# Kernel tuning notes

Hardware: AMD Instinct MI355X
Metric: run time of the kernel (lower is better)

Reference implementation:

```python
import jax, jax.numpy as jnp
import numpy as np

DIM = 512
HEADS = 8
HEAD_DIM = DIM // HEADS
EPS = 1e-5

def _ln(x, g, b):
    m = jnp.mean(x, axis=-1, keepdims=True)
    v = jnp.mean((x - m) ** 2, axis=-1, keepdims=True)
    return (x - m) * jax.lax.rsqrt(v + EPS) * g + b

def setup_inputs() -> dict:
    key = jax.random.key(0)
    ks = jax.random.split(key, 12)
    s = 0.02
    d, dff = DIM, 4 * DIM
    inp = {
        'x': jax.random.normal(ks[0], (8, 4096, d), jnp.float32),
        'Wq': jax.random.normal(ks[1], (d, d), jnp.float32) * s,
        'bq': jnp.zeros((d,), jnp.float32),
        'Wk': jax.random.normal(ks[2], (d, d), jnp.float32) * s,
        'bk': jnp.zeros((d,), jnp.float32),
        'Wv': jax.random.normal(ks[3], (d, d), jnp.float32) * s,
        'bv': jnp.zeros((d,), jnp.float32),
        'Wo': jax.random.normal(ks[4], (d, d), jnp.float32) * s,
        'bo': jnp.zeros((d,), jnp.float32),
        'g1': jnp.ones((d,), jnp.float32),
        'b1': jnp.zeros((d,), jnp.float32),
        'g2': jnp.ones((d,), jnp.float32),
        'b2': jnp.zeros((d,), jnp.float32),
        'Wf1': jax.random.normal(ks[5], (d, dff), jnp.float32) * s,
        'bf1': jnp.zeros((dff,), jnp.float32),
        'Wf2': jax.random.normal(ks[6], (dff, d), jnp.float32) * s,
        'bf2': jnp.zeros((d,), jnp.float32),
    }
    return inp

def _linear_attn(x, Wq, bq, Wk, bk, Wv, bv, Wo, bo):
    b, n, d = x.shape
    def split(t):
        return t.reshape(b, n, HEADS, HEAD_DIM).transpose(0, 2, 1, 3)  # bhnd
    q = split(x @ Wq + bq)
    k = split(x @ Wk + bk)
    v = split(x @ Wv + bv)
    q = jax.nn.elu(q) + 1.0
    k = jax.nn.elu(k) + 1.0
    kv = jnp.einsum('bhnd,bhnf->bhdf', k, v)
    out = jnp.einsum('bhnd,bhdf->bhnf', q, kv)
    out = out.transpose(0, 2, 1, 3).reshape(b, n, d)
    return out @ Wo + bo

def reference(x, Wq, bq, Wk, bk, Wv, bv, Wo, bo, g1, b1, g2, b2, Wf1, bf1, Wf2, bf2):
    # series decomposition: AvgPool1d(k=3, stride=1, pad=1, count_include_pad=True)
    xp = jnp.pad(x, ((0, 0), (1, 1), (0, 0)))
    trend = (xp[:, :-2] + xp[:, 1:-1] + xp[:, 2:]) / 3.0
    seasonal = x - trend
    seasonal = seasonal + _linear_attn(_ln(seasonal, g1, b1), Wq, bq, Wk, bk, Wv, bv, Wo, bo)
    h = _ln(seasonal, g2, b2)
    h = jax.nn.gelu(h @ Wf1 + bf1, approximate=False) @ Wf2 + bf2
    seasonal = seasonal + h
    return seasonal + trend
```

## Files before the change

### kernel.cpp

```cpp
#include <hip/hip_runtime.h>
#include <math.h>

typedef __bf16 bf16;
typedef __attribute__((ext_vector_type(8))) __bf16 bf16x8;
typedef __attribute__((ext_vector_type(4))) float floatx4;

#define DIM 512
#define DFF 2048
#define SEQ 4096
#define ROWS 32768

#define GLOBAL_AS(p) ((const __attribute__((address_space(1))) void*)(p))
#define LDS_AS(p)    ((__attribute__((address_space(3))) void*)(p))

__global__ __launch_bounds__(256) void prep_w_kernel(const float* __restrict__ W,
                                                     bf16* __restrict__ Wt, int K, int N)
{
    int idx = blockIdx.x * 256 + threadIdx.x;
    if (idx >= K * N) return;
    int k = idx % K;
    int n = idx / K;
    Wt[idx] = (bf16)W[(size_t)k * N + n];
}

__global__ __launch_bounds__(256) void prep_w3_kernel(const float* __restrict__ Wq,
                                                      const float* __restrict__ Wk,
                                                      const float* __restrict__ Wv,
                                                      bf16* __restrict__ Wt)
{
    int idx = blockIdx.x * 256 + threadIdx.x;
    int which = idx >> 18;
    int r = idx & 262143;
    int k = r & 511;
    int n = r >> 9;
    const float* W = (which == 0) ? Wq : (which == 1 ? Wk : Wv);
    Wt[idx] = (bf16)W[(size_t)k * 512 + n];
}

__global__ __launch_bounds__(256) void pack_bias_kernel(const float* __restrict__ bq,
                                                        const float* __restrict__ bk,
                                                        const float* __restrict__ bv,
                                                        float* __restrict__ out)
{
    int i = blockIdx.x * 256 + threadIdx.x;
    if (i >= 1536) return;
    out[i] = (i < 512) ? bq[i] : (i < 1024 ? bk[i - 512] : bv[i - 1024]);
}

__device__ inline float wave_red(float v)
{
#pragma unroll
    for (int off = 32; off; off >>= 1) v += __shfl_xor(v, off, 64);
    return v;
}

__global__ __launch_bounds__(256) void decomp_ln_kernel(const float* __restrict__ x,
                                                        const float* __restrict__ g,
                                                        const float* __restrict__ be,
                                                        float* __restrict__ S,
                                                        bf16* __restrict__ XN)
{
    int wave = threadIdx.x >> 6, lane = threadIdx.x & 63;
    int r = blockIdx.x * 4 + wave;
    int n = r & (SEQ - 1);
    const float4* xr = (const float4*)(x + (size_t)r * DIM);
    float4 z = make_float4(0.f, 0.f, 0.f, 0.f);
    float s[8];
#pragma unroll
    for (int i = 0; i < 2; ++i) {
        int c4 = lane * 2 + i;
        float4 v0 = xr[c4];
        float4 vm = (n > 0)       ? xr[c4 - DIM / 4] : z;
        float4 vp = (n < SEQ - 1) ? xr[c4 + DIM / 4] : z;
        s[i * 4 + 0] = v0.x - (vm.x + v0.x + vp.x) * (1.f / 3.f);
        s[i * 4 + 1] = v0.y - (vm.y + v0.y + vp.y) * (1.f / 3.f);
        s[i * 4 + 2] = v0.z - (vm.z + v0.z + vp.z) * (1.f / 3.f);
        s[i * 4 + 3] = v0.w - (vm.w + v0.w + vp.w) * (1.f / 3.f);
    }
    float4* Sr = (float4*)(S + (size_t)r * DIM);
    Sr[lane * 2]     = make_float4(s[0], s[1], s[2], s[3]);
    Sr[lane * 2 + 1] = make_float4(s[4], s[5], s[6], s[7]);

    float sum = 0.f;
#pragma unroll
    for (int j = 0; j < 8; ++j) sum += s[j];
    sum = wave_red(sum);
    float mean = sum * (1.f / DIM);
    float vs = 0.f;
#pragma unroll
    for (int j = 0; j < 8; ++j) { float d = s[j] - mean; vs += d * d; }
    vs = wave_red(vs);
    float rstd = rsqrtf(vs * (1.f / DIM) + 1e-5f);

    int c = lane * 8;
    float4 g0 = ((const float4*)(g + c))[0],  g1v = ((const float4*)(g + c))[1];
    float4 b0 = ((const float4*)(be + c))[0], b1v = ((const float4*)(be + c))[1];
    bf16x8 o;
    o[0] = (bf16)((s[0] - mean) * rstd * g0.x + b0.x);
    o[1] = (bf16)((s[1] - mean) * rstd * g0.y + b0.y);
    o[2] = (bf16)((s[2] - mean) * rstd * g0.z + b0.z);
    o[3] = (bf16)((s[3] - mean) * rstd * g0.w + b0.w);
    o[4] = (bf16)((s[4] - mean) * rstd * g1v.x + b1v.x);
    o[5] = (bf16)((s[5] - mean) * rstd * g1v.y + b1v.y);
    o[6] = (bf16)((s[6] - mean) * rstd * g1v.z + b1v.z);
    o[7] = (bf16)((s[7] - mean) * rstd * g1v.w + b1v.w);
    *(bf16x8*)(XN + (size_t)r * DIM + c) = o;
}

__global__ __launch_bounds__(256) void ln_kernel(const float* __restrict__ X,
                                                 const float* __restrict__ g,
                                                 const float* __restrict__ be,
                                                 bf16* __restrict__ XN)
{
    int wave = threadIdx.x >> 6, lane = threadIdx.x & 63;
    int r = blockIdx.x * 4 + wave;
    const float4* xr = (const float4*)(X + (size_t)r * DIM);
    float4 a0 = xr[lane * 2], a1 = xr[lane * 2 + 1];
    float s[8] = {a0.x, a0.y, a0.z, a0.w, a1.x, a1.y, a1.z, a1.w};
    float sum = 0.f;
#pragma unroll
    for (int j = 0; j < 8; ++j) sum += s[j];
    sum = wave_red(sum);
    float mean = sum * (1.f / DIM);
    float vs = 0.f;
#pragma unroll
    for (int j = 0; j < 8; ++j) { float d = s[j] - mean; vs += d * d; }
    vs = wave_red(vs);
    float rstd = rsqrtf(vs * (1.f / DIM) + 1e-5f);
    int c = lane * 8;
    float4 g0 = ((const float4*)(g + c))[0],  g1v = ((const float4*)(g + c))[1];
    float4 b0 = ((const float4*)(be + c))[0], b1v = ((const float4*)(be + c))[1];
    bf16x8 o;
    o[0] = (bf16)((s[0] - mean) * rstd * g0.x + b0.x);
    o[1] = (bf16)((s[1] - mean) * rstd * g0.y + b0.y);
    o[2] = (bf16)((s[2] - mean) * rstd * g0.z + b0.z);
    o[3] = (bf16)((s[3] - mean) * rstd * g0.w + b0.w);
    o[4] = (bf16)((s[4] - mean) * rstd * g1v.x + b1v.x);
    o[5] = (bf16)((s[5] - mean) * rstd * g1v.y + b1v.y);
    o[6] = (bf16)((s[6] - mean) * rstd * g1v.z + b1v.z);
    o[7] = (bf16)((s[7] - mean) * rstd * g1v.w + b1v.w);
    *(bf16x8*)(XN + (size_t)r * DIM + c) = o;
}

enum { M_QKV = 0, M_ATTN = 1, M_FFN1 = 2, M_FFN2 = 3 };

template <int MODE>
__global__ __launch_bounds__(512, 2) void gemm_bt_kernel(const bf16* __restrict__ A, int lda,
                                                         const bf16* __restrict__ Bt,
                                                         const float* __restrict__ bias,
                                                         float* S, const float* __restrict__ X,
                                                         void* Cout, int ldc,
                                                         int N, int K, int rows_per_batch,
                                                         int m_off)
{
    __shared__ __align__(16) bf16 lA[3][256 * 32];
    __shared__ __align__(16) bf16 lB[3][256 * 32];
    int tid = threadIdx.x;

    int nwg = gridDim.x * gridDim.y;
    int orig = blockIdx.y * gridDim.x + blockIdx.x;
    int wg = (orig & 7) * (nwg >> 3) + (orig >> 3);
    int m0 = (wg / gridDim.x) * 256;
    int n0 = (wg % gridDim.x) * 256;

    const bf16* Abase = A + (size_t)m0 * lda;
    const bf16* Bbase = Bt + (size_t)n0 * K;
    if (rows_per_batch) Bbase += (size_t)(m0 / rows_per_batch) * (size_t)N * K;

    int lane = tid & 63;
    int wave = tid >> 6;
    int wm = (wave >> 2) * 128;
    int wn = (wave & 3) * 64;
    int lm = lane & 15;
    int quad = lane >> 4;
    int ebase = tid & 448;

    floatx4 acc[8][4];
#pragma unroll
    for (int i = 0; i < 8; ++i)
#pragma unroll
        for (int j = 0; j < 4; ++j) acc[i][j] = (floatx4){0.f, 0.f, 0.f, 0.f};

    auto stage = [&](int buf, int k0) {
#pragma unroll
        for (int l = 0; l < 2; ++l) {
            int e  = l * 512 + tid;
            int eb = l * 512 + ebase;
            int row = e >> 2;
            int col = ((e & 3) ^ (row & 3)) * 8;
            __builtin_amdgcn_global_load_lds(GLOBAL_AS(Abase + (size_t)row * lda + k0 + col),
                                             LDS_AS(&lA[buf][eb * 8]), 16, 0, 0);
            __builtin_amdgcn_global_load_lds(GLOBAL_AS(Bbase + (size_t)row * K + k0 + col),
                                             LDS_AS(&lB[buf][eb * 8]), 16, 0, 0);
        }
    };

    stage(0, 0);
    stage(1, 32);
    asm volatile("s_waitcnt vmcnt(4)" ::: "memory");
    __builtin_amdgcn_s_barrier();

    int nsteps = K >> 5;
    int cur = 0;
    for (int s = 0; s < nsteps; ++s) {
        bf16x8 af[8], bfv[4];
#pragma unroll
        for (int i = 0; i < 8; ++i) {
            int ra = wm + i * 16 + lm;
            af[i] = *(const bf16x8*)&lA[cur][ra * 32 + (quad ^ (ra & 3)) * 8];
        }
#pragma unroll
        for (int j = 0; j < 4; ++j) {
            int rb = wn + j * 16 + lm;
            bfv[j] = *(const bf16x8*)&lB[cur][rb * 32 + (quad ^ (rb & 3)) * 8];
        }

        int kpre = (s + 2) << 5;
        bool issued = kpre < K;
        if (issued) {
            int nxt = cur + 2; if (nxt >= 3) nxt -= 3;
            stage(nxt, kpre);
        }

#pragma unroll
        for (int i = 0; i < 8; ++i)
#pragma unroll
            for (int j = 0; j < 4; ++j)
                acc[i][j] = __builtin_amdgcn_mfma_f32_16x16x32_bf16(af[i], bfv[j], acc[i][j], 0, 0, 0);

        if (issued) asm volatile("s_waitcnt vmcnt(4)" ::: "memory");
        else        asm volatile("s_waitcnt vmcnt(0)" ::: "memory");
        __builtin_amdgcn_s_barrier();
        cur = (cur == 2) ? 0 : cur + 1;
    }

#pragma unroll
    for (int i = 0; i < 8; ++i) {
        int gm_base = m0 + wm + i * 16 + quad * 4;
#pragma unroll
        for (int j = 0; j < 4; ++j) {
            int gn = n0 + wn + j * 16 + lm;
            float bia = bias[gn];
            if constexpr (MODE == M_FFN2) {
                int gmg0 = m_off + gm_base;
                int bn = gmg0 & (SEQ - 1);
                size_t ob = (size_t)gmg0 * DIM + gn;
                const float* Xb = X + ob;
                float xr6[6];
#pragma unroll
                for (int r = 0; r < 6; ++r) {
                    int nr = bn + r - 1;
                    xr6[r] = (nr >= 0 && nr < SEQ) ? Xb[(long)(r - 1) * DIM] : 0.f;
                }
                float* op = (float*)Cout;
#pragma unroll
                for (int e = 0; e < 4; ++e) {
                    size_t o = ob + (size_t)e * DIM;
                    float val = acc[i][j][e] + bia;
                    op[o] = val + op[o] + (xr6[e] + xr6[e + 1] + xr6[e + 2]) * (1.f / 3.f);
                }
            } else {
#pragma unroll
                for (int e = 0; e < 4; ++e) {
                    int gm = gm_base + e;
                    float val = acc[i][j][e] + bia;
                    if constexpr (MODE == M_QKV) {
                        if (gn < 1024) val = (val > 0.f) ? val + 1.f : __expf(val);
                        ((bf16*)Cout)[(size_t)gm * ldc + gn] = (bf16)val;
                    } else if constexpr (MODE == M_ATTN) {
                        S[(size_t)gm * DIM + gn] += val;
                    } else {
                        val = 0.5f * val * (1.f + erff(val * 0.70710678118654752f));
                        ((bf16*)Cout)[(size_t)gm * ldc + gn] = (bf16)val;
                    }
                }
            }
        }
    }
}

__global__ __launch_bounds__(256) void kv_mfma_kernel(const bf16* __restrict__ QKV,
                                                      float* __restrict__ KV)
{
    int kc = blockIdx.x, h = blockIdx.y, b = blockIdx.z;
    __shared__ __align__(16) bf16 lbuf[3][2 * 128 * 64];
    int tid = threadIdx.x;
    int lane = tid & 63, wave = tid >> 6;
    int lm = lane & 15, quad = lane >> 4;

    floatx4 acc[4][4];
#pragma unroll
    for (int i = 0; i < 4; ++i)
#pragma unroll
        for (int j = 0; j < 4; ++j) acc[i][j] = (floatx4){0.f, 0.f, 0.f, 0.f};

    const bf16* kb = QKV + (size_t)b * SEQ * 1536 + 512 + (size_t)h * 64;
    const bf16* vb = kb + 512;
    int drow = lane >> 3;
    int d0 = (lane & 7) * 8;

    auto stage = [&](int buf, int it) {
        int n0 = kc * 1024 + it * 128;
#pragma unroll
        for (int q = 0; q < 4; ++q) {
            int nbase = wave * 32 + q * 8;
            int ldsoff = wave * 2048 + q * 512;
            __builtin_amdgcn_global_load_lds(GLOBAL_AS(kb + (size_t)(n0 + nbase + drow) * 1536 + d0),
                                             LDS_AS(&lbuf[buf][ldsoff]), 16, 0, 0);
            __builtin_amdgcn_global_load_lds(GLOBAL_AS(vb + (size_t)(n0 + nbase + drow) * 1536 + d0),
                                             LDS_AS(&lbuf[buf][8192 + ldsoff]), 16, 0, 0);
        }
    };

    stage(0, 0);
    stage(1, 1);
    asm volatile("s_waitcnt vmcnt(8)" ::: "memory");
    __builtin_amdgcn_s_barrier();

    int cur = 0;
    for (int it = 0; it < 8; ++it) {
        const bf16* lk = lbuf[cur];
        const bf16* lv = lbuf[cur] + 8192;
        int nw = wave * 32 + quad * 8;
        bf16x8 af[4], bfv[4];
#pragma unroll
        for (int i = 0; i < 4; ++i) {
            int dd = i * 16 + lm;
#pragma unroll
            for (int j = 0; j < 8; ++j) af[i][j] = lk[(nw + j) * 64 + dd];
#pragma unroll
            for (int j = 0; j < 8; ++j) bfv[i][j] = lv[(nw + j) * 64 + dd];
        }

        bool issued = (it + 2) < 8;
        if (issued) {
            int nxt = cur + 2; if (nxt >= 3) nxt -= 3;
            stage(nxt, it + 2);
        }

#pragma unroll
        for (int i = 0; i < 4; ++i)
#pragma unroll
            for (int j = 0; j < 4; ++j)
                acc[i][j] = __builtin_amdgcn_mfma_f32_16x16x32_bf16(af[i], bfv[j], acc[i][j], 0, 0, 0);

        if (issued) asm volatile("s_waitcnt vmcnt(8)" ::: "memory");
        else        asm volatile("s_waitcnt vmcnt(0)" ::: "memory");
        __builtin_amdgcn_s_barrier();
        cur = (cur == 2) ? 0 : cur + 1;
    }

    __syncthreads();
    float* red = (float*)lbuf;
    if (wave < 2) {
#pragma unroll
        for (int i = 0; i < 4; ++i)
#pragma unroll
            for (int j = 0; j < 4; ++j)
#pragma unroll
                for (int e = 0; e < 4; ++e)
                    red[wave * 4096 + (i * 16 + quad * 4 + e) * 64 + j * 16 + lm] = acc[i][j][e];
    }
    __syncthreads();
    if (wave >= 2) {
#pragma unroll
        for (int i = 0; i < 4; ++i)
#pragma unroll
            for (int j = 0; j < 4; ++j)
#pragma unroll
                for (int e = 0; e < 4; ++e)
                    red[(wave - 2) * 4096 + (i * 16 + quad * 4 + e) * 64 + j * 16 + lm] += acc[i][j][e];
    }
    __syncthreads();
    float* dst = KV + ((size_t)kc * 64 + b * 8 + h) * 4096;
#pragma unroll
    for (int p = 0; p < 4; ++p) {
        int e4 = (tid + p * 256) * 4;
        float4 a = *(const float4*)&red[e4];
        float4 c4 = *(const float4*)&red[4096 + e4];
        a.x += c4.x; a.y += c4.y; a.z += c4.z; a.w += c4.w;
        *(float4*)&dst[e4] = a;
    }
}

__global__ __launch_bounds__(256) void kvw_kernel(const float* __restrict__ KV,
                                                  const float* __restrict__ Wo,
                                                  bf16* __restrict__ KVWT)
{
    int jc = blockIdx.x & 7, bh = blockIdx.x >> 3;
    int h = bh & 7, b = bh >> 3;
    __shared__ float skvT[64 * 68];
    int tid = threadIdx.x;
    const float* src = KV + (size_t)bh * 4096;
#pragma unroll
    for (int p = 0; p < 16; ++p) {
        int e = tid + p * 256;
        float s = src[e] + src[e + 262144] + src[e + 524288] + src[e + 786432];
        skvT[(e & 63) * 68 + (e >> 6)] = s;
    }
    __syncthreads();

    int j = tid & 63, dq = tid >> 6;
    int j0 = jc * 64;
    floatx4 acc4[4];
#pragma unroll
    for (int c = 0; c < 4; ++c) acc4[c] = (floatx4){0.f, 0.f, 0.f, 0.f};
    const float* wop = Wo + (size_t)h * 64 * 512 + j0 + j;
#pragma unroll 8
    for (int f = 0; f < 64; ++f) {
        float w = wop[(size_t)f * 512];
        const float* sp = &skvT[f * 68 + dq * 16];
#pragma unroll
        for (int c = 0; c < 4; ++c) {
            floatx4 s = *(const floatx4*)(sp + c * 4);
            acc4[c] += s * w;
        }
    }
    bf16* dst = KVWT + (size_t)b * 262144 + (size_t)(j0 + j) * 512 + h * 64 + dq * 16;
    bf16x8 o0, o1;
#pragma unroll
    for (int t = 0; t < 8; ++t) { o0[t] = (bf16)acc4[t >> 2][t & 3]; o1[t] = (bf16)acc4[2 + (t >> 2)][t & 3]; }
    *(bf16x8*)dst = o0;
    *(bf16x8*)(dst + 8) = o1;
}

extern "C" void kernel_launch(void* const* d_in, const int* in_sizes, int n_in,
                              void* d_out, int out_size, void* d_ws, size_t ws_size,
                              hipStream_t stream)
{
    const float* x   = (const float*)d_in[0];
    const float* Wq  = (const float*)d_in[1];
    const float* bq  = (const float*)d_in[2];
    const float* Wk  = (const float*)d_in[3];
    const float* bk  = (const float*)d_in[4];
    const float* Wv  = (const float*)d_in[5];
    const float* bv  = (const float*)d_in[6];
    const float* Wo  = (const float*)d_in[7];
    const float* bo  = (const float*)d_in[8];
    const float* g1  = (const float*)d_in[9];
    const float* b1  = (const float*)d_in[10];
    const float* g2  = (const float*)d_in[11];
    const float* b2  = (const float*)d_in[12];
    const float* Wf1 = (const float*)d_in[13];
    const float* bf1 = (const float*)d_in[14];
    const float* Wf2 = (const float*)d_in[15];
    const float* bf2 = (const float*)d_in[16];
    float* out = (float*)d_out;
    (void)in_sizes; (void)n_in; (void)out_size;

    char* ws = (char*)d_ws;
    size_t off = 0;
    auto alloc = [&](size_t bytes) -> char* {
        char* p = ws + off;
        off += (bytes + 255) & ~(size_t)255;
        return p;
    };
    bf16*  WqkvT = (bf16*)alloc((size_t)1536 * 512 * 2);
    float* bias3 = (float*)alloc(1536 * 4);
    bf16*  Wf1T  = (bf16*)alloc((size_t)2048 * 512 * 2);
    bf16*  Wf2T  = (bf16*)alloc((size_t)512 * 2048 * 2);
    size_t post_xn_off = 0;
    bf16*  XN    = (bf16*)alloc((size_t)ROWS * DIM * 2);
    post_xn_off = off;
    float* KV    = (float*)alloc((size_t)4 * 64 * 4096 * 4);
    bf16*  KVWT  = (bf16*)alloc((size_t)8 * 512 * 512 * 2);
    bf16*  QKV   = (bf16*)alloc((size_t)ROWS * 1536 * 2);

    size_t h1_bytes  = (size_t)ROWS * DFF * 2;
    bool   merged    = ws_size >= post_xn_off + h1_bytes;
    bf16*  H1full    = (bf16*)(ws + post_xn_off);
    bf16*  H1chunk   = QKV;

    prep_w3_kernel<<<3072, 256, 0, stream>>>(Wq, Wk, Wv, WqkvT);
    prep_w_kernel<<<4096, 256, 0, stream>>>(Wf1, Wf1T, 512, 2048);
    prep_w_kernel<<<4096, 256, 0, stream>>>(Wf2, Wf2T, 2048, 512);
    pack_bias_kernel<<<6, 256, 0, stream>>>(bq, bk, bv, bias3);

    decomp_ln_kernel<<<8192, 256, 0, stream>>>(x, g1, b1, out, XN);

    gemm_bt_kernel<M_QKV><<<dim3(6, 128), 512, 0, stream>>>(
        XN, 512, WqkvT, bias3, nullptr, nullptr, QKV, 1536, 1536, 512, 0, 0);

    kv_mfma_kernel<<<dim3(4, 8, 8), 256, 0, stream>>>(QKV, KV);

    kvw_kernel<<<512, 256, 0, stream>>>(KV, Wo, KVWT);

    gemm_bt_kernel<M_ATTN><<<dim3(2, 128), 512, 0, stream>>>(
        QKV, 1536, KVWT, bo, out, nullptr, nullptr, 0, 512, 512, 4096, 0);

    ln_kernel<<<8192, 256, 0, stream>>>(out, g2, b2, XN);

    if (merged) {
        gemm_bt_kernel<M_FFN1><<<dim3(8, 128), 512, 0, stream>>>(
            XN, 512, Wf1T, bf1, nullptr, nullptr, H1full, 2048, 2048, 512, 0, 0);
        gemm_bt_kernel<M_FFN2><<<dim3(2, 128), 512, 0, stream>>>(
            H1full, 2048, Wf2T, bf2, nullptr, x, out, 512, 512, 2048, 0, 0);
    } else {
        for (int c = 0; c < 2; ++c) {
            gemm_bt_kernel<M_FFN1><<<dim3(8, 64), 512, 0, stream>>>(
                XN + (size_t)c * 16384 * 512, 512, Wf1T, bf1, nullptr, nullptr,
                H1chunk, 2048, 2048, 512, 0, 0);
            gemm_bt_kernel<M_FFN2><<<dim3(2, 64), 512, 0, stream>>>(
                H1chunk, 2048, Wf2T, bf2, nullptr, x, out, 512, 512, 2048, 0, c * 16384);
        }
    }
}
```

Measured before the change: 616.7 us.

## Restructure GEMM main loop into ping-pong 64-wide K tiles with staged prefetch

Replaces the triple-buffered 32-wide K pipeline with double-buffered 64-wide K tiles. Each tile is split into four MFMA sub-phases, and the global-to-LDS loads for the next tiles are interleaved between them. s_setprio raises the priority of the MFMA blocks, and explicit barriers and waitcnts schedule the overlap. The goal is fewer barriers per K element and better overlap of memory with matrix math. In exchange, the loop needs more barriers per tile and the LDS footprint grows (128KB), which may limit occupancy.

Measured after the change: 636.6 us. 1.03x slower.

```diff
diff --git a/kernel.cpp b/kernel.cpp
--- a/kernel.cpp
+++ b/kernel.cpp
@@ -12,6 +12,11 @@
 
 #define GLOBAL_AS(p) ((const __attribute__((address_space(1))) void*)(p))
 #define LDS_AS(p)    ((__attribute__((address_space(3))) void*)(p))
+
+#define BARX()  __builtin_amdgcn_s_barrier()
+#define LGKM0() do { asm volatile("s_waitcnt lgkmcnt(0)" ::: "memory"); \
+                     __builtin_amdgcn_sched_barrier(0); } while (0)
+#define VMW(n)  asm volatile("s_waitcnt vmcnt(" #n ")" ::: "memory")
 
 __global__ __launch_bounds__(256) void prep_w_kernel(const float* __restrict__ W,
                                                      bf16* __restrict__ Wt, int K, int N)
@@ -153,8 +158,8 @@
                                                          int N, int K, int rows_per_batch,
                                                          int m_off)
 {
-    __shared__ __align__(16) bf16 lA[3][256 * 32];
-    __shared__ __align__(16) bf16 lB[3][256 * 32];
+    __shared__ __align__(16) bf16 lAa[256 * 64], lAb[256 * 64];
+    __shared__ __align__(16) bf16 lBa[256 * 64], lBb[256 * 64];
     int tid = threadIdx.x;
 
     int nwg = gridDim.x * gridDim.y;
@@ -169,11 +174,10 @@
 
     int lane = tid & 63;
     int wave = tid >> 6;
-    int wm = (wave >> 2) * 128;
-    int wn = (wave & 3) * 64;
-    int lm = lane & 15;
+    int wmp  = (wave >> 2) * 128;
+    int wn   = (wave & 3) * 64;
+    int lm   = lane & 15;
     int quad = lane >> 4;
-    int ebase = tid & 448;
 
     floatx4 acc[8][4];
 #pragma unroll
@@ -181,62 +185,82 @@
 #pragma unroll
         for (int j = 0; j < 4; ++j) acc[i][j] = (floatx4){0.f, 0.f, 0.f, 0.f};
 
-    auto stage = [&](int buf, int k0) {
-#pragma unroll
-        for (int l = 0; l < 2; ++l) {
-            int e  = l * 512 + tid;
-            int eb = l * 512 + ebase;
-            int row = e >> 2;
-            int col = ((e & 3) ^ (row & 3)) * 8;
-            __builtin_amdgcn_global_load_lds(GLOBAL_AS(Abase + (size_t)row * lda + k0 + col),
-                                             LDS_AS(&lA[buf][eb * 8]), 16, 0, 0);
-            __builtin_amdgcn_global_load_lds(GLOBAL_AS(Bbase + (size_t)row * K + k0 + col),
-                                             LDS_AS(&lB[buf][eb * 8]), 16, 0, 0);
-        }
-    };
-
-    stage(0, 0);
-    stage(1, 32);
-    asm volatile("s_waitcnt vmcnt(4)" ::: "memory");
-    __builtin_amdgcn_s_barrier();
-
-    int nsteps = K >> 5;
-    int cur = 0;
-    for (int s = 0; s < nsteps; ++s) {
-        bf16x8 af[8], bfv[4];
-#pragma unroll
-        for (int i = 0; i < 8; ++i) {
-            int ra = wm + i * 16 + lm;
-            af[i] = *(const bf16x8*)&lA[cur][ra * 32 + (quad ^ (ra & 3)) * 8];
-        }
+    auto stq = [&](bf16* arr, const bf16* mat, int ld, int kt, int q) {
+        int r = q * 64 + (tid >> 3);
+        int g = tid & 7;
+        __builtin_amdgcn_global_load_lds(
+            GLOBAL_AS(mat + (size_t)r * ld + kt * 64 + ((g ^ (r & 7)) * 8)),
+            LDS_AS(arr + q * 4096 + tid * 8), 16, 0, 0);
+    };
+    auto rdA = [&](const bf16* arr, int half, int kk, bf16x8* a) {
+#pragma unroll
+        for (int i = 0; i < 4; ++i) {
+            int r = wmp + half * 64 + i * 16 + lm;
+            a[i] = *(const bf16x8*)&arr[r * 64 + (((kk * 4 + quad) ^ (r & 7)) * 8)];
+        }
+    };
+    auto rdB = [&](const bf16* arr, int kk, bf16x8* b) {
 #pragma unroll
         for (int j = 0; j < 4; ++j) {
-            int rb = wn + j * 16 + lm;
-            bfv[j] = *(const bf16x8*)&lB[cur][rb * 32 + (quad ^ (rb & 3)) * 8];
-        }
-
-        int kpre = (s + 2) << 5;
-        bool issued = kpre < K;
-        if (issued) {
-            int nxt = cur + 2; if (nxt >= 3) nxt -= 3;
-            stage(nxt, kpre);
-        }
-
-#pragma unroll
-        for (int i = 0; i < 8; ++i)
+            int r = wn + j * 16 + lm;
+            b[j] = *(const bf16x8*)&arr[r * 64 + (((kk * 4 + quad) ^ (r & 7)) * 8)];
+        }
+    };
+    auto mf = [&](int ioff, bf16x8* a, bf16x8* b) {
+        __builtin_amdgcn_s_setprio(1);
+#pragma unroll
+        for (int i = 0; i < 4; ++i)
 #pragma unroll
             for (int j = 0; j < 4; ++j)
-                acc[i][j] = __builtin_amdgcn_mfma_f32_16x16x32_bf16(af[i], bfv[j], acc[i][j], 0, 0, 0);
-
-        if (issued) asm volatile("s_waitcnt vmcnt(4)" ::: "memory");
-        else        asm volatile("s_waitcnt vmcnt(0)" ::: "memory");
-        __builtin_amdgcn_s_barrier();
-        cur = (cur == 2) ? 0 : cur + 1;
-    }
+                acc[ioff + i][j] =
+                    __builtin_amdgcn_mfma_f32_16x16x32_bf16(a[i], b[j], acc[ioff + i][j], 0, 0, 0);
+        __builtin_amdgcn_s_setprio(0);
+    };
+
+    auto tile4 = [&](const bf16* Ac, const bf16* Bc, bf16* An, bf16* Bn, bf16* Bcm,
+                     int u, bool s1, bool s2) {
+        bf16x8 a[4], b0[4], b1[4];
+        rdA(Ac, 0, 0, a);
+        rdB(Bc, 0, b0);
+        if (s1) { stq(Bn, Bbase, K, u + 1, 2); stq(Bn, Bbase, K, u + 1, 3); }
+        BARX(); LGKM0(); mf(0, a, b0);
+        if (s1) { VMW(4); } else { VMW(0); }
+        BARX();
+        rdA(Ac, 1, 0, a);
+        if (s1) { stq(An, Abase, lda, u + 1, 0); stq(An, Abase, lda, u + 1, 2); }
+        BARX(); LGKM0(); mf(4, a, b0);
+        BARX();
+        rdA(Ac, 0, 1, a);
+        rdB(Bc, 1, b1);
+        if (s1) { stq(An, Abase, lda, u + 1, 1); stq(An, Abase, lda, u + 1, 3); }
+        BARX(); LGKM0(); mf(0, a, b1);
+        BARX();
+        rdA(Ac, 1, 1, a);
+        if (s2) { stq(Bcm, Bbase, K, u + 2, 0); stq(Bcm, Bbase, K, u + 2, 1); }
+        BARX(); LGKM0(); mf(4, a, b1);
+        if (s2) { VMW(4); } else if (s1) { VMW(2); }
+        BARX();
+    };
+
+    stq(lBa, Bbase, K, 0, 0); stq(lBa, Bbase, K, 0, 1);
+    stq(lBa, Bbase, K, 0, 2); stq(lBa, Bbase, K, 0, 3);
+    stq(lAa, Abase, lda, 0, 0); stq(lAa, Abase, lda, 0, 2);
+    stq(lAa, Abase, lda, 0, 1); stq(lAa, Abase, lda, 0, 3);
+    stq(lBb, Bbase, K, 1, 0); stq(lBb, Bbase, K, 1, 1);
+    VMW(4);
+    BARX();
+
+    int T = K >> 6;
+    for (int u = 0; u + 3 < T; u += 2) {
+        tile4(lAa, lBa, lAb, lBb, lBa, u,     true, true);
+        tile4(lAb, lBb, lAa, lBa, lBb, u + 1, true, true);
+    }
+    tile4(lAa, lBa, lAb, lBb, lBa, T - 2, true,  false);
+    tile4(lAb, lBb, lAa, lBa, lBb, T - 1, false, false);
 
 #pragma unroll
     for (int i = 0; i < 8; ++i) {
-        int gm_base = m0 + wm + i * 16 + quad * 4;
+        int gm_base = m0 + wmp + i * 16 + quad * 4;
 #pragma unroll
         for (int j = 0; j < 4; ++j) {
             int gn = n0 + wn + j * 16 + lm;
```
